# Performance work log

Hardware: AMD Instinct MI355X
Metric: run time of the kernel (lower is better)

Reference implementation:

```python
import jax, jax.numpy as jnp
import numpy as np

B, S, D_IN, D_EMB, H = 2, 2048, 1024, 1024, 16
HD = D_EMB // H  # projection_dim = 64


def setup_inputs() -> dict:
    key = jax.random.key(0)
    ks = jax.random.split(key, 9)
    s_in = 1.0 / np.sqrt(D_IN)
    s_emb = 1.0 / np.sqrt(D_EMB)
    return {
        "inputs": jax.random.normal(ks[0], (B, S, D_IN), dtype=jnp.float32),
        "Wq": jax.random.uniform(ks[1], (D_IN, D_EMB), jnp.float32, -s_in, s_in),
        "bq": jax.random.uniform(ks[2], (D_EMB,), jnp.float32, -s_in, s_in),
        "Wk": jax.random.uniform(ks[3], (D_IN, D_EMB), jnp.float32, -s_in, s_in),
        "bk": jax.random.uniform(ks[4], (D_EMB,), jnp.float32, -s_in, s_in),
        "Wv": jax.random.uniform(ks[5], (D_IN, D_EMB), jnp.float32, -s_in, s_in),
        "bv": jax.random.uniform(ks[6], (D_EMB,), jnp.float32, -s_in, s_in),
        "Wo": jax.random.uniform(ks[7], (D_EMB, D_EMB), jnp.float32, -s_emb, s_emb),
        "bo": jax.random.uniform(ks[8], (D_EMB,), jnp.float32, -s_emb, s_emb),
    }


def reference(inputs, Wq, bq, Wk, bk, Wv, bv, Wo, bo):
    b, s, _ = inputs.shape
    # QKV projections -> [b, h, s, hd]
    def split_heads(x):
        return x.reshape(b, s, H, HD).transpose(0, 2, 1, 3)
    q = split_heads(inputs @ Wq + bq)
    k = split_heads(inputs @ Wk + bk)
    v = split_heads(inputs @ Wv + bv)
    scale = 1.0 / jnp.sqrt(jnp.float32(HD))
    logits = jnp.einsum('bhqd,bhkd->bhqk', q, k) * scale
    attn = jax.nn.softmax(logits, axis=-1)
    ctx = jnp.einsum('bhqk,bhkd->bhqd', attn, v)  # [b,h,s,hd]
    concat = ctx.transpose(0, 2, 1, 3).reshape(b, s, D_EMB)
    return concat @ Wo + bo
```

## Files before the change

kernel.cpp:

```cpp
#include <hip/hip_runtime.h>
#include <stdint.h>

#define S_ 2048
#define H_ 16

typedef short s16x8 __attribute__((ext_vector_type(8)));
typedef float f32x4 __attribute__((ext_vector_type(4)));
typedef float f32x16 __attribute__((ext_vector_type(16)));

__device__ __forceinline__ ushort f2bf(float f) {
    union { float f; uint32_t u; } v; v.f = f;
    uint32_t r = v.u + 0x7fffu + ((v.u >> 16) & 1u);
    return (ushort)(r >> 16);
}
__device__ __forceinline__ uint32_t cvtpk(float a, float b) {
    uint32_t r;
    asm("v_cvt_pk_bf16_f32 %0, %1, %2" : "=v"(r) : "v"(a), "v"(b));
    return r;
}
__device__ __forceinline__ void plswap(uint32_t& a, uint32_t& b) {
    auto r = __builtin_amdgcn_permlane32_swap((int)a, (int)b, false, false);
    a = (uint32_t)r[0];
    b = (uint32_t)r[1];
}
__device__ __forceinline__ float xmax32(float x) {
    uint32_t a = __float_as_uint(x), b = a;
    plswap(a, b);
    return fmaxf(__uint_as_float(a), __uint_as_float(b));
}
__device__ __forceinline__ float xadd32(float x) {
    uint32_t a = __float_as_uint(x), b = a;
    plswap(a, b);
    return __uint_as_float(a) + __uint_as_float(b);
}
__device__ __forceinline__ float exp2_fast(float x) {
    float r;
    asm("v_exp_f32 %0, %1" : "=v"(r) : "v"(x));
    return r;
}

__device__ __forceinline__ void gld16(ushort* lds, const ushort* g) {
    auto* gp = reinterpret_cast<uint32_t __attribute__((address_space(1)))*>(
        reinterpret_cast<uintptr_t>(g));
    auto* lp = reinterpret_cast<uint32_t __attribute__((address_space(3)))*>(
        reinterpret_cast<uintptr_t>(lds));
    __builtin_amdgcn_global_load_lds(gp, lp, 16, 0, 0);
}

__global__ void cast_bf16(const float* __restrict__ src, ushort* __restrict__ dst) {
    size_t i = ((size_t)blockIdx.x * 256 + threadIdx.x) * 8;
    float4 x = *(const float4*)(src + i);
    float4 y = *(const float4*)(src + i + 4);
    s16x8 r;
    r[0] = (short)f2bf(x.x); r[1] = (short)f2bf(x.y);
    r[2] = (short)f2bf(x.z); r[3] = (short)f2bf(x.w);
    r[4] = (short)f2bf(y.x); r[5] = (short)f2bf(y.y);
    r[6] = (short)f2bf(y.z); r[7] = (short)f2bf(y.w);
    *(s16x8*)(dst + i) = r;
}

__global__ void transpose_k4(const float* __restrict__ s0, const float* __restrict__ s1,
                             const float* __restrict__ s2, const float* __restrict__ s3,
                             ushort* __restrict__ d0, ushort* __restrict__ d1,
                             ushort* __restrict__ d2, ushort* __restrict__ d3) {
    const int z = blockIdx.z;
    const float* src = (z == 0) ? s0 : (z == 1) ? s1 : (z == 2) ? s2 : s3;
    ushort* dst      = (z == 0) ? d0 : (z == 1) ? d1 : (z == 2) ? d2 : d3;
    __shared__ ushort t[32][33];
    int bx = blockIdx.x * 32, by = blockIdx.y * 32;
    int x = threadIdx.x;
    for (int y = threadIdx.y; y < 32; y += 8)
        t[y][x] = f2bf(src[(size_t)(by + y) * 1024 + bx + x]);
    __syncthreads();
    for (int y = threadIdx.y; y < 32; y += 8)
        dst[(size_t)(bx + y) * 1024 + by + x] = t[x][y];
}

#define MFMA16(a, b, c) __builtin_amdgcn_mfma_f32_16x16x32_bf16(a, b, c, 0, 0, 0)

__global__ __launch_bounds__(256, 4) void gemm_bt(
        const ushort* __restrict__ A,
        const ushort* __restrict__ Bt0, const ushort* __restrict__ Bt1,
        const ushort* __restrict__ Bt2,
        const float* __restrict__ bi0, const float* __restrict__ bi1,
        const float* __restrict__ bi2,
        void* __restrict__ o0, void* __restrict__ o1, void* __restrict__ o2,
        int mode0) {
    const int z = blockIdx.z;
    const ushort* Bt  = (z == 0) ? Bt0 : (z == 1) ? Bt1 : Bt2;
    const float* bia  = (z == 0) ? bi0 : (z == 1) ? bi1 : bi2;
    void* out         = (z == 0) ? o0  : (z == 1) ? o1  : o2;
    const int mode = mode0 + z;

    __shared__ __align__(16) ushort Asm[128 * 64];
    __shared__ __align__(16) ushort Bsm[128 * 64];

    const int t = threadIdx.x;
    const int lane = t & 63, w = t >> 6;
    const int wm = w >> 1, wn = w & 1;
    const int quad = lane >> 4, l16 = lane & 15;

    const int bid = blockIdx.y * 8 + blockIdx.x;
    const int swz = (bid & 7) * 32 + (bid >> 3);
    const int m0 = (swz >> 3) * 128, n0 = (swz & 7) * 128;
    const int K = 1024;

    const f32x4 FZ = {0.f, 0.f, 0.f, 0.f};
    f32x4 acc[4][4];
#pragma unroll
    for (int i = 0; i < 4; i++)
#pragma unroll
        for (int j = 0; j < 4; j++) acc[i][j] = FZ;

    const int rr = t >> 3;
    const int sc = (t & 7) ^ (rr & 7);
    const ushort* Ap = A  + (size_t)(m0 + rr) * K + sc * 8;
    const ushort* Bp = Bt + (size_t)(n0 + rr) * K + sc * 8;
    ushort* AsmW = Asm + w * 512;
    ushort* BsmW = Bsm + w * 512;

    const int fx = l16 & 7;

    for (int kt = 0; kt < 16; ++kt) {
        __syncthreads();
        const int o = kt * 64;
#pragma unroll
        for (int g = 0; g < 4; g++) {
            gld16(AsmW + g * 2048, Ap + (size_t)(g * 32) * K + o);
            gld16(BsmW + g * 2048, Bp + (size_t)(g * 32) * K + o);
        }
        __syncthreads();

#pragma unroll
        for (int ks = 0; ks < 2; ks++) {
            const int ck = (((ks << 2) | quad) ^ fx) * 8;
            s16x8 a[4], b[4];
#pragma unroll
            for (int i = 0; i < 4; i++)
                a[i] = *(const s16x8*)&Asm[(wm * 64 + i * 16 + l16) * 64 + ck];
#pragma unroll
            for (int j = 0; j < 4; j++)
                b[j] = *(const s16x8*)&Bsm[(wn * 64 + j * 16 + l16) * 64 + ck];
#pragma unroll
            for (int i = 0; i < 4; i++)
#pragma unroll
                for (int j = 0; j < 4; j++)
                    acc[i][j] = MFMA16(a[i], b[j], acc[i][j]);
        }
    }

    if (mode == 3) {
        ushort* T = Asm;
        const int b_ = m0 >> 11;
        const int s_base = m0 & 2047;
        __syncthreads();
#pragma unroll
        for (int half = 0; half < 2; ++half) {
            if (wn == half) {
#pragma unroll
                for (int j = 0; j < 4; j++) {
                    int nl = j * 16 + l16;
                    float bv = bia[n0 + half * 64 + nl];
#pragma unroll
                    for (int i = 0; i < 4; i++) {
#pragma unroll
                        for (int r = 0; r < 4; r++) {
                            int ml = wm * 64 + i * 16 + quad * 4 + r;
                            T[nl * 128 + (ml ^ ((nl & 15) << 3))] = f2bf(acc[i][j][r] + bv);
                        }
                    }
                }
            }
            __syncthreads();
            {
                int row = t >> 2, cg = (t & 3) * 32;
                int ng = n0 + half * 64 + row;
                int h = ng >> 6, d = ng & 63;
                ushort* op = (ushort*)out + ((size_t)((b_ * 16 + h) * 64 + d)) * 2048 + s_base + cg;
#pragma unroll
                for (int c = 0; c < 4; c++) {
                    int col = (cg + c * 8) ^ ((row & 15) << 3);
                    *(s16x8*)(op + c * 8) = *(const s16x8*)(T + row * 128 + col);
                }
            }
            __syncthreads();
        }
        return;
    }

#pragma unroll
    for (int j = 0; j < 4; j++) {
        int n = n0 + wn * 64 + j * 16 + l16;
        float bv = bia[n];
#pragma unroll
        for (int i = 0; i < 4; i++) {
#pragma unroll
            for (int r = 0; r < 4; r++) {
                int m = m0 + wm * 64 + i * 16 + quad * 4 + r;
                float v = acc[i][j][r] + bv;
                if (mode == 0) {
                    ((float*)out)[(size_t)m * 1024 + n] = v;
                } else {
                    int b_ = m >> 11, s = m & 2047;
                    int h = n >> 6, d = n & 63;
                    if (mode == 1)
                        ((ushort*)out)[((size_t)(b_ * 16 + h) * 2048 + s) * 64 + d] = f2bf(v * 0.18033688011112042f);
                    else
                        ((ushort*)out)[((size_t)(b_ * 16 + h) * 2048 + s) * 64 + d] = f2bf(v);
                }
            }
        }
    }
}

#define MFMA32(a, b, c) __builtin_amdgcn_mfma_f32_32x32x16_bf16(a, b, c, 0, 0, 0)

__global__ __launch_bounds__(256, 2) void attn(const ushort* __restrict__ q_ws,
                                               const ushort* __restrict__ k_ws,
                                               const ushort* __restrict__ vt_ws,
                                               ushort* __restrict__ ctx) {
    __shared__ __align__(16) ushort SM[3 * 8192];

    const int t = threadIdx.x, lane = t & 63, w = t >> 6;
    const int l32 = lane & 31, hi = lane >> 5;

    const int bid = blockIdx.x;
    const int j_ = bid >> 3;
    const int bh = (bid & 7) + 8 * (j_ >> 4);
    const int q0 = (j_ & 15) * 128 + w * 32;

    const ushort* Qg = q_ws + (size_t)bh * S_ * 64;
    const ushort* Kg = k_ws + (size_t)bh * S_ * 64;
    const ushort* Vg = vt_ws + (size_t)bh * 64 * S_;

    s16x8 qf[4];
#pragma unroll
    for (int dc = 0; dc < 4; dc++)
        qf[dc] = *(const s16x8*)&Qg[(size_t)(q0 + l32) * 64 + dc * 16 + hi * 8];

    const int sr = t >> 3;
    const int sc = (t & 7) ^ (sr & 7);
    const ushort* kS = Kg + sr * 64 + sc * 8;
    const ushort* vS = Vg + (size_t)sr * 2048 + sc * 8;

#define STG(bufidx, kt) do {                                        \
    ushort* dK = SM + (bufidx) * 8192 + w * 512;                    \
    const ushort* kn = kS + (size_t)(kt) * 4096;                    \
    const ushort* vn = vS + (kt) * 64;                              \
    gld16(dK,               kn);                                    \
    gld16(dK + 2048,        kn + 2048);                             \
    gld16(dK + 4096,        vn);                                    \
    gld16(dK + 4096 + 2048, vn + (size_t)32 * 2048);                \
} while (0)

    int fo[4];
#pragma unroll
    for (int c = 0; c < 4; c++)
        fo[c] = l32 * 64 + ((((c << 1) | hi) ^ (l32 & 7)) << 3);

    const f32x16 Z16 = {0.f,0.f,0.f,0.f,0.f,0.f,0.f,0.f,0.f,0.f,0.f,0.f,0.f,0.f,0.f,0.f};
    f32x16 o0 = Z16, o1 = Z16;
    float m_run = -1e30f, l_run = 0.f;

    STG(0, 0);
    STG(1, 1);

    int cb = 0, nb = 2;
    for (int kt = 0; kt < S_ / 64; ++kt) {
        if (kt == S_ / 64 - 1) asm volatile("s_waitcnt vmcnt(0)" ::: "memory");
        else                   asm volatile("s_waitcnt vmcnt(4)" ::: "memory");
        __builtin_amdgcn_s_barrier();
        __builtin_amdgcn_sched_barrier(0);
        if (kt < S_ / 64 - 2) STG(nb, kt + 2);

        const ushort* KB = SM + cb * 8192;
        const ushort* VB = KB + 4096;

        f32x16 s0 = Z16, s1 = Z16;
        __builtin_amdgcn_s_setprio(1);
#pragma unroll
        for (int dc = 0; dc < 4; dc++) {
            s16x8 k0 = *(const s16x8*)(KB + fo[dc]);
            s16x8 k1 = *(const s16x8*)(KB + 2048 + fo[dc]);
            s0 = MFMA32(k0, qf[dc], s0);
            s1 = MFMA32(k1, qf[dc], s1);
        }
        __builtin_amdgcn_s_setprio(0);

        float m0 = fmaxf(s0[0], s1[0]), m1 = fmaxf(s0[1], s1[1]);
        float m2 = fmaxf(s0[2], s1[2]), m3 = fmaxf(s0[3], s1[3]);
#pragma unroll
        for (int r = 4; r < 16; r += 4) {
            m0 = fmaxf(m0, fmaxf(s0[r],     s1[r]));
            m1 = fmaxf(m1, fmaxf(s0[r + 1], s1[r + 1]));
            m2 = fmaxf(m2, fmaxf(s0[r + 2], s1[r + 2]));
            m3 = fmaxf(m3, fmaxf(s0[r + 3], s1[r + 3]));
        }
        float mx = fmaxf(fmaxf(m0, m1), fmaxf(m2, m3));
        mx = xmax32(mx);

        if (__any(mx > m_run + 8.f)) {
            float mnew = fmaxf(m_run, mx);
            float alpha = exp2_fast(m_run - mnew);
            m_run = mnew;
            l_run *= alpha;
#pragma unroll
            for (int r = 0; r < 16; r++) { o0[r] *= alpha; o1[r] *= alpha; }
        }

        float ra = 0.f, rb = 0.f;
#pragma unroll
        for (int r = 0; r < 16; r++) {
            s0[r] = exp2_fast(s0[r] - m_run); ra += s0[r];
            s1[r] = exp2_fast(s1[r] - m_run); rb += s1[r];
        }
        l_run += xadd32(ra + rb);

#pragma unroll
        for (int ks = 0; ks < 2; ks++) {
            const f32x16& p = ks ? s1 : s0;
            uint32_t u0 = cvtpk(p[0], p[1]),   u2 = cvtpk(p[4], p[5]);
            plswap(u0, u2);
            uint32_t u1 = cvtpk(p[2], p[3]),   u3 = cvtpk(p[6], p[7]);
            plswap(u1, u3);
            uint32_t w0 = cvtpk(p[8], p[9]),   w2 = cvtpk(p[12], p[13]);
            plswap(w0, w2);
            uint32_t w1 = cvtpk(p[10], p[11]), w3 = cvtpk(p[14], p[15]);
            plswap(w1, w3);
            union { uint32_t u[4]; s16x8 h; } F0, F1;
            F0.u[0] = u0; F0.u[1] = u1; F0.u[2] = u2; F0.u[3] = u3;
            F1.u[0] = w0; F1.u[1] = w1; F1.u[2] = w2; F1.u[3] = w3;

            const int kc0 = ks * 2, kc1 = ks * 2 + 1;
            s16x8 v00 = *(const s16x8*)(VB + fo[kc0]);
            s16x8 v01 = *(const s16x8*)(VB + 2048 + fo[kc0]);
            s16x8 v10 = *(const s16x8*)(VB + fo[kc1]);
            s16x8 v11 = *(const s16x8*)(VB + 2048 + fo[kc1]);
            __builtin_amdgcn_s_setprio(1);
            o0 = MFMA32(v00, F0.h, o0); o1 = MFMA32(v01, F0.h, o1);
            o0 = MFMA32(v10, F1.h, o0); o1 = MFMA32(v11, F1.h, o1);
            __builtin_amdgcn_s_setprio(0);
        }

        asm volatile("s_waitcnt lgkmcnt(0)" ::: "memory");
        cb = (cb == 2) ? 0 : cb + 1;
        nb = (nb == 2) ? 0 : nb + 1;
    }
#undef STG

    ushort* obuf = SM;
    float inv = 1.0f / l_run;
    const int ob = (w * 32 + l32) * 72;
#pragma unroll
    for (int r = 0; r < 16; r++) {
        int d0 = (r & 3) + 8 * (r >> 2) + 4 * hi;
        obuf[ob + d0]      = f2bf(o0[r] * inv);
        obuf[ob + 32 + d0] = f2bf(o1[r] * inv);
    }
    asm volatile("s_waitcnt lgkmcnt(0)" ::: "memory");
    __builtin_amdgcn_sched_barrier(0);
    int b_ = bh >> 4, h = bh & 15;
    ushort* gp = ctx + ((size_t)(b_ * 2048 + q0 + l32)) * 1024 + h * 64 + hi * 32;
#pragma unroll
    for (int c = 0; c < 4; c++)
        *(s16x8*)(gp + c * 8) = *(const s16x8*)&obuf[ob + hi * 32 + c * 8];
}

extern "C" void kernel_launch(void* const* d_in, const int* in_sizes, int n_in,
                              void* d_out, int out_size, void* d_ws, size_t ws_size,
                              hipStream_t stream) {
    const float* X  = (const float*)d_in[0];
    const float* Wq = (const float*)d_in[1];
    const float* bq = (const float*)d_in[2];
    const float* Wk = (const float*)d_in[3];
    const float* bk = (const float*)d_in[4];
    const float* Wv = (const float*)d_in[5];
    const float* bv = (const float*)d_in[6];
    const float* Wo = (const float*)d_in[7];
    const float* bo = (const float*)d_in[8];
    float* out = (float*)d_out;

    char* ws = (char*)d_ws;
    ushort* wtq  = (ushort*)(ws);
    ushort* wtk  = (ushort*)(ws + ((size_t)2 << 20));
    ushort* wtv  = (ushort*)(ws + ((size_t)4 << 20));
    ushort* wto  = (ushort*)(ws + ((size_t)6 << 20));
    ushort* qws  = (ushort*)(ws + ((size_t)8 << 20));
    ushort* kws  = (ushort*)(ws + ((size_t)16 << 20));
    ushort* ctx  = (ushort*)(ws + ((size_t)24 << 20));
    ushort* vtws = (ushort*)d_out;
    ushort* xbf  = (ushort*)d_out + ((size_t)4 << 20);

    transpose_k4<<<dim3(32, 32, 4), dim3(32, 8), 0, stream>>>(Wq, Wk, Wv, Wo,
                                                              wtq, wtk, wtv, wto);
    cast_bf16<<<2048, 256, 0, stream>>>(X, xbf);

    gemm_bt<<<dim3(8, 32, 3), 256, 0, stream>>>(xbf, wtq, wtk, wtv, bq, bk, bv,
                                                qws, kws, vtws, 1);

    attn<<<dim3(512), 256, 0, stream>>>(qws, kws, vtws, ctx);

    gemm_bt<<<dim3(8, 32, 1), 256, 0, stream>>>(ctx, wto, wto, wto, bo, bo, bo,
                                                out, out, out, 0);
}
```

Before: 202.6 us.

## Triple-buffer GEMM K-loop with async LDS loads and merge prep kernels

Rewrites the GEMM main loop from a two-barrier, single-buffer K=64 step into a three-stage ring of K=32 LDS buffers. Global-to-LDS loads for step kt+2 are issued while step kt computes, with a vmcnt wait, one barrier per step, and raised priority around the MFMAs. The aim is to hide global load latency behind compute, at the cost of more LDS per block (occupancy hint lowered to 3 blocks) and a new swizzle. The weight transpose and input cast are also fused into one launch to save a kernel launch.

```diff
diff --git a/kernel.cpp b/kernel.cpp
--- a/kernel.cpp
+++ b/kernel.cpp
@@ -47,38 +47,42 @@
     __builtin_amdgcn_global_load_lds(gp, lp, 16, 0, 0);
 }
 
-__global__ void cast_bf16(const float* __restrict__ src, ushort* __restrict__ dst) {
-    size_t i = ((size_t)blockIdx.x * 256 + threadIdx.x) * 8;
-    float4 x = *(const float4*)(src + i);
-    float4 y = *(const float4*)(src + i + 4);
-    s16x8 r;
-    r[0] = (short)f2bf(x.x); r[1] = (short)f2bf(x.y);
-    r[2] = (short)f2bf(x.z); r[3] = (short)f2bf(x.w);
-    r[4] = (short)f2bf(y.x); r[5] = (short)f2bf(y.y);
-    r[6] = (short)f2bf(y.z); r[7] = (short)f2bf(y.w);
-    *(s16x8*)(dst + i) = r;
-}
-
-__global__ void transpose_k4(const float* __restrict__ s0, const float* __restrict__ s1,
-                             const float* __restrict__ s2, const float* __restrict__ s3,
-                             ushort* __restrict__ d0, ushort* __restrict__ d1,
-                             ushort* __restrict__ d2, ushort* __restrict__ d3) {
+__global__ void prep(const float* __restrict__ s0, const float* __restrict__ s1,
+                     const float* __restrict__ s2, const float* __restrict__ s3,
+                     const float* __restrict__ X,
+                     ushort* __restrict__ d0, ushort* __restrict__ d1,
+                     ushort* __restrict__ d2, ushort* __restrict__ d3,
+                     ushort* __restrict__ xdst) {
     const int z = blockIdx.z;
-    const float* src = (z == 0) ? s0 : (z == 1) ? s1 : (z == 2) ? s2 : s3;
-    ushort* dst      = (z == 0) ? d0 : (z == 1) ? d1 : (z == 2) ? d2 : d3;
-    __shared__ ushort t[32][33];
-    int bx = blockIdx.x * 32, by = blockIdx.y * 32;
-    int x = threadIdx.x;
-    for (int y = threadIdx.y; y < 32; y += 8)
-        t[y][x] = f2bf(src[(size_t)(by + y) * 1024 + bx + x]);
-    __syncthreads();
-    for (int y = threadIdx.y; y < 32; y += 8)
-        dst[(size_t)(bx + y) * 1024 + by + x] = t[x][y];
+    if (z < 4) {
+        const float* src = (z == 0) ? s0 : (z == 1) ? s1 : (z == 2) ? s2 : s3;
+        ushort* dst      = (z == 0) ? d0 : (z == 1) ? d1 : (z == 2) ? d2 : d3;
+        __shared__ ushort t[32][33];
+        int bx = blockIdx.x * 32, by = blockIdx.y * 32;
+        int x = threadIdx.x;
+        for (int y = threadIdx.y; y < 32; y += 8)
+            t[y][x] = f2bf(src[(size_t)(by + y) * 1024 + bx + x]);
+        __syncthreads();
+        for (int y = threadIdx.y; y < 32; y += 8)
+            dst[(size_t)(bx + y) * 1024 + by + x] = t[x][y];
+    } else {
+        int bl = (z - 4) * 1024 + blockIdx.y * 32 + blockIdx.x;
+        int tl = threadIdx.y * 32 + threadIdx.x;
+        size_t i = ((size_t)bl * 256 + tl) * 8;
+        float4 x = *(const float4*)(X + i);
+        float4 y = *(const float4*)(X + i + 4);
+        s16x8 r;
+        r[0] = (short)f2bf(x.x); r[1] = (short)f2bf(x.y);
+        r[2] = (short)f2bf(x.z); r[3] = (short)f2bf(x.w);
+        r[4] = (short)f2bf(y.x); r[5] = (short)f2bf(y.y);
+        r[6] = (short)f2bf(y.z); r[7] = (short)f2bf(y.w);
+        *(s16x8*)(xdst + i) = r;
+    }
 }
 
 #define MFMA16(a, b, c) __builtin_amdgcn_mfma_f32_16x16x32_bf16(a, b, c, 0, 0, 0)
 
-__global__ __launch_bounds__(256, 4) void gemm_bt(
+__global__ __launch_bounds__(256, 3) void gemm_bt(
         const ushort* __restrict__ A,
         const ushort* __restrict__ Bt0, const ushort* __restrict__ Bt1,
         const ushort* __restrict__ Bt2,
@@ -92,8 +96,7 @@
     void* out         = (z == 0) ? o0  : (z == 1) ? o1  : o2;
     const int mode = mode0 + z;
 
-    __shared__ __align__(16) ushort Asm[128 * 64];
-    __shared__ __align__(16) ushort Bsm[128 * 64];
+    __shared__ __align__(16) ushort SM[3 * 8192];
 
     const int t = threadIdx.x;
     const int lane = t & 63, w = t >> 6;
@@ -112,45 +115,60 @@
 #pragma unroll
         for (int j = 0; j < 4; j++) acc[i][j] = FZ;
 
-    const int rr = t >> 3;
-    const int sc = (t & 7) ^ (rr & 7);
+    const int rr = t >> 2;
+    const int sc = (t & 3) ^ ((t >> 3) & 3);
     const ushort* Ap = A  + (size_t)(m0 + rr) * K + sc * 8;
     const ushort* Bp = Bt + (size_t)(n0 + rr) * K + sc * 8;
-    ushort* AsmW = Asm + w * 512;
-    ushort* BsmW = Bsm + w * 512;
-
-    const int fx = l16 & 7;
-
-    for (int kt = 0; kt < 16; ++kt) {
-        __syncthreads();
-        const int o = kt * 64;
-#pragma unroll
-        for (int g = 0; g < 4; g++) {
-            gld16(AsmW + g * 2048, Ap + (size_t)(g * 32) * K + o);
-            gld16(BsmW + g * 2048, Bp + (size_t)(g * 32) * K + o);
-        }
-        __syncthreads();
-
-#pragma unroll
-        for (int ks = 0; ks < 2; ks++) {
-            const int ck = (((ks << 2) | quad) ^ fx) * 8;
-            s16x8 a[4], b[4];
-#pragma unroll
-            for (int i = 0; i < 4; i++)
-                a[i] = *(const s16x8*)&Asm[(wm * 64 + i * 16 + l16) * 64 + ck];
+
+#define STG(bufidx, kt) do {                                        \
+    ushort* dA = SM + (bufidx) * 8192 + w * 512;                    \
+    const int _o = (kt) * 32;                                       \
+    gld16(dA,               Ap + _o);                               \
+    gld16(dA + 2048,        Ap + (size_t)64 * K + _o);              \
+    gld16(dA + 4096,        Bp + _o);                               \
+    gld16(dA + 4096 + 2048, Bp + (size_t)64 * K + _o);              \
+} while (0)
+
+    const int fx2 = (l16 >> 1) & 3;
+    const int ck = (quad ^ fx2) * 8;
+
+    STG(0, 0);
+    STG(1, 1);
+
+    int cb = 0, nb = 2;
+    for (int kt = 0; kt < 32; ++kt) {
+        if (kt == 31) asm volatile("s_waitcnt vmcnt(0)" ::: "memory");
+        else          asm volatile("s_waitcnt vmcnt(4)" ::: "memory");
+        __builtin_amdgcn_s_barrier();
+        __builtin_amdgcn_sched_barrier(0);
+        if (kt < 30) STG(nb, kt + 2);
+
+        const ushort* Ab = SM + cb * 8192;
+        const ushort* Bb = Ab + 4096;
+
+        s16x8 a[4], b[4];
+#pragma unroll
+        for (int i = 0; i < 4; i++)
+            a[i] = *(const s16x8*)&Ab[(wm * 64 + i * 16 + l16) * 32 + ck];
+#pragma unroll
+        for (int j = 0; j < 4; j++)
+            b[j] = *(const s16x8*)&Bb[(wn * 64 + j * 16 + l16) * 32 + ck];
+        __builtin_amdgcn_s_setprio(1);
+#pragma unroll
+        for (int i = 0; i < 4; i++)
 #pragma unroll
             for (int j = 0; j < 4; j++)
-                b[j] = *(const s16x8*)&Bsm[(wn * 64 + j * 16 + l16) * 64 + ck];
-#pragma unroll
-            for (int i = 0; i < 4; i++)
-#pragma unroll
-                for (int j = 0; j < 4; j++)
-                    acc[i][j] = MFMA16(a[i], b[j], acc[i][j]);
-        }
-    }
+                acc[i][j] = MFMA16(a[i], b[j], acc[i][j]);
+        __builtin_amdgcn_s_setprio(0);
+
+        asm volatile("s_waitcnt lgkmcnt(0)" ::: "memory");
+        cb = (cb == 2) ? 0 : cb + 1;
+        nb = (nb == 2) ? 0 : nb + 1;
+    }
+#undef STG
 
     if (mode == 3) {
-        ushort* T = Asm;
+        ushort* T = SM;
         const int b_ = m0 >> 11;
         const int s_base = m0 & 2047;
         __syncthreads();
@@ -391,9 +409,8 @@
     ushort* vtws = (ushort*)d_out;
     ushort* xbf  = (ushort*)d_out + ((size_t)4 << 20);
 
-    transpose_k4<<<dim3(32, 32, 4), dim3(32, 8), 0, stream>>>(Wq, Wk, Wv, Wo,
-                                                              wtq, wtk, wtv, wto);
-    cast_bf16<<<2048, 256, 0, stream>>>(X, xbf);
+    prep<<<dim3(32, 32, 6), dim3(32, 8), 0, stream>>>(Wq, Wk, Wv, Wo, X,
+                                                      wtq, wtk, wtv, wto, xbf);
 
     gemm_bt<<<dim3(8, 32, 3), 256, 0, stream>>>(xbf, wtq, wtk, wtv, bq, bk, bv,
                                                 qws, kws, vtws, 1);
```

Result: faster. 197.8 us (-2.4%).
